# Kernel optimization log

Measured on AMD Instinct MI355X. Metric: run time of the kernel, lower is better.

Reference implementation:

```python
import jax, jax.numpy as jnp
import numpy as np

B, N, T = 8192, 100, 64  # batch, ROI nodes, BOLD timepoints/features
GCN_DIMS = [(T, 32), (32, 16), (16, 8), (8, 4), (4, 2)]
EPS = 1e-5


def _kaiming(key, fout, fin):
    return jax.random.normal(key, (fout, fin), jnp.float32) * np.float32(np.sqrt(2.0 / fin))


def setup_inputs() -> dict:
    key = jax.random.key(0)
    ks = jax.random.split(key, 10)
    inp = {"BOLD_signals": jax.random.normal(ks[0], (B, N, T), jnp.float32)}
    inp["Wq"] = _kaiming(ks[1], 32, 64); inp["bq"] = jnp.zeros((32,), jnp.float32)
    inp["Wk"] = _kaiming(ks[2], 32, 64); inp["bk"] = jnp.zeros((32,), jnp.float32)
    inp["Wv"] = _kaiming(ks[3], 32, 64); inp["bv"] = jnp.zeros((32,), jnp.float32)
    for i, (fin, fout) in enumerate(GCN_DIMS):
        inp[f"W{i+1}"] = _kaiming(ks[4 + i], fout, fin)
        inp[f"b{i+1}"] = jnp.zeros((fout,), jnp.float32)
    inp["Wf"] = _kaiming(ks[9], 2, 200); inp["bf"] = jnp.zeros((2,), jnp.float32)
    return inp


def _corrcoef_batched(feat):
    # feat: [B, N, D]; rows are variables -> [B, N, N] correlation (torch.corrcoef, clipped)
    xc = feat - feat.mean(axis=-1, keepdims=True)
    cov = jnp.einsum('bnd,bmd->bnm', xc, xc)  # unnormalized; divisor cancels
    d = jnp.sqrt(jnp.einsum('bnn->bn', cov))
    corr = cov / (d[:, :, None] * d[:, None, :])
    return jnp.clip(corr, -1.0, 1.0)


def _batchnorm_nodes(h):
    # BatchNorm1d(100) on [B, 100, C]: normalize per node over (batch, feature) dims;
    # gamma=1, beta=0 per the module's constant init; training-mode batch stats.
    mean = h.mean(axis=(0, 2), keepdims=True)
    var = ((h - mean) ** 2).mean(axis=(0, 2), keepdims=True)
    return (h - mean) * jax.lax.rsqrt(var + EPS)


def _gcn(corr, h, W, b):
    z = jnp.einsum('bnm,bmf->bnf', corr, h) @ W.T + b
    return jnp.tanh(_batchnorm_nodes(z))


def reference(BOLD_signals, Wq, bq, Wk, bk, Wv, bv,
              W1, b1, W2, b2, W3, b3, W4, b4, W5, b5, Wf, bf):
    x = BOLD_signals
    Q = x @ Wq.T + bq
    K = x @ Wk.T + bk
    V = x @ Wv.T + bv
    A = jax.nn.softmax(jnp.einsum('bnd,bmd->bnm', Q, K) / 32.0, axis=2)
    feat = jnp.einsum('bnm,bmd->bnd', A, V)  # [B, N, 32]
    corr = _corrcoef_batched(feat)           # [B, N, N]
    h = x
    for (W, b) in [(W1, b1), (W2, b2), (W3, b3), (W4, b4), (W5, b5)]:
        h = _gcn(corr, h, W, b)
    out = h.reshape(h.shape[0], -1) @ Wf.T + bf  # [B, 2]
    return out
```

## Files before the change

kernel.cpp:

```cpp
#include <hip/hip_runtime.h>
#include <hip/hip_bf16.h>


typedef unsigned int u32;
typedef unsigned short u16;
typedef float f32x4 __attribute__((ext_vector_type(4)));
typedef short s16x8 __attribute__((ext_vector_type(8)));

__device__ __forceinline__ f32x4 mfma16(s16x8 a, s16x8 b, f32x4 c) {
  return __builtin_amdgcn_mfma_f32_16x16x32_bf16(a, b, c, 0, 0, 0);
}
__device__ __forceinline__ u16 f2b(float f) {
  __hip_bfloat16 h = __float2bfloat16(f);
  u16 u; __builtin_memcpy(&u, &h, 2); return u;
}
__device__ __forceinline__ float b2f(u16 u) { return __uint_as_float((u32)u << 16); }
__device__ __forceinline__ float blo(u32 u) { return __uint_as_float(u << 16); }
__device__ __forceinline__ float bhi(u32 u) { return __uint_as_float(u & 0xffff0000u); }
__device__ __forceinline__ u32 pack_hi2(float a, float b) { return (u32)f2b(a) | ((u32)f2b(b) << 16); }
__device__ __forceinline__ u32 pack_lo2(float a, float b) {
  return (u32)f2b(a - b2f(f2b(a))) | ((u32)f2b(b - b2f(f2b(b))) << 16);
}
__device__ __forceinline__ float fast_tanh(float x) {
  float e = __expf(2.0f * x);
  return 1.0f - 2.0f * __builtin_amdgcn_rcpf(e + 1.0f);
}

#define KA_XHI_B   0
#define KA_XLO_B   16128
#define KA_A_B     0
#define KA_QS_B    32256
#define KA_KS_B    40320
#define KA_CHH_B   32256
#define KA_CHL_B   40320
#define KA_VT_B    48384
#define KA_CRH_B   0
#define KA_CRL_B   30464
#define KA_T0H_B   60928
#define KA_T0L_B   69632
#define KA_SMEM_B  78336

__global__ __launch_bounds__(512, 4) void ka_kernel(
    const float* __restrict__ x,
    const float* __restrict__ Wq, const float* __restrict__ bq,
    const float* __restrict__ Wk, const float* __restrict__ bk,
    const float* __restrict__ Wv, const float* __restrict__ bv,
    const float* __restrict__ W1, const float* __restrict__ b1,
    __hip_bfloat16* __restrict__ corr_g,
    float* __restrict__ z1g,
    float* __restrict__ stats1)
{
  __shared__ __align__(16) char smem[KA_SMEM_B];
  u16* xh  = (u16*)(smem + KA_XHI_B);
  u16* xl  = (u16*)(smem + KA_XLO_B);
  u16* A16 = (u16*)(smem + KA_A_B);
  u16* Qs  = (u16*)(smem + KA_QS_B);
  u16* Ks  = (u16*)(smem + KA_KS_B);
  u16* chh = (u16*)(smem + KA_CHH_B);
  u16* chl = (u16*)(smem + KA_CHL_B);
  u16* Vt  = (u16*)(smem + KA_VT_B);
  u16* crh = (u16*)(smem + KA_CRH_B);
  u16* crl = (u16*)(smem + KA_CRL_B);
  u16* t0h = (u16*)(smem + KA_T0H_B);
  u16* t0l = (u16*)(smem + KA_T0L_B);

  const int b = blockIdx.x, tid = threadIdx.x;
  const int w = tid >> 6, l15 = tid & 15, g = (tid & 63) >> 4;
  const f32x4 zero4 = {0.f, 0.f, 0.f, 0.f};

  float t0r[28];
  float cr[7][4];

  {
    const float2* xg2 = (const float2*)(x + (size_t)b * 6400);
    for (int i = tid; i < 112 * 32; i += 512) {
      int r = i >> 5, c2 = i & 31;
      float vx = 0.f, vy = 0.f;
      if (r < 100) { float2 v = xg2[r * 32 + c2]; vx = v.x; vy = v.y; }
      ((u32*)xh)[r * 36 + c2] = pack_hi2(vx, vy);
      ((u32*)xl)[r * 36 + c2] = pack_lo2(vx, vy);
    }
    if (tid < 256) {
      int j = tid >> 3, ii = tid & 7;
      ((u32*)Vt)[j * 68 + 56 + ii] = 0;
    }
  }
  __syncthreads();

  {
    const int mi = w >> 1, half = w & 1;
    const int j = 16 * half + l15;
    const float* Wp = (mi == 0) ? Wq : (mi == 1) ? Wk : (mi == 2) ? Wv : W1;
    float bias = (mi == 0) ? bq[j] : (mi == 1) ? bk[j] : (mi == 2) ? bv[j] : 0.f;
    s16x8 bhf[2], blf[2];
#pragma unroll
    for (int kt = 0; kt < 2; ++kt) {
      const float* wr = Wp + j * 64 + kt * 32 + g * 8;
#pragma unroll
      for (int e = 0; e < 8; ++e) {
        float wv = wr[e];
        u16 hh = f2b(wv);
        bhf[kt][e] = (short)hh;
        blf[kt][e] = (short)f2b(wv - b2f(hh));
      }
    }
#pragma unroll
    for (int tm = 0; tm < 7; ++tm) {
      f32x4 acc = zero4;
#pragma unroll
      for (int kt = 0; kt < 2; ++kt) {
        s16x8 ah = *(const s16x8*)&xh[(16 * tm + l15) * 72 + kt * 32 + g * 8];
        s16x8 al = *(const s16x8*)&xl[(16 * tm + l15) * 72 + kt * 32 + g * 8];
        acc = mfma16(al, bhf[kt], acc);
        acc = mfma16(ah, blf[kt], acc);
        acc = mfma16(ah, bhf[kt], acc);
      }
      const int row0 = 16 * tm + 4 * g;
#pragma unroll
      for (int r = 0; r < 4; ++r) {
        int row = row0 + r;
        float v = acc[r] + bias;
        if (mi == 0)      Qs[row * 36 + j] = f2b(v);
        else if (mi == 1) Ks[row * 36 + j] = f2b(v);
        else if (mi == 2) Vt[j * 136 + row] = f2b(v);
        else              t0r[tm * 4 + r] = v;
      }
    }
  }
  __syncthreads();

  if (w < 7) {
    const int tm = w;
    s16x8 aq = *(const s16x8*)&Qs[(16 * tm + l15) * 36 + g * 8];
    f32x4 sc[7];
#pragma unroll
    for (int tn = 0; tn < 7; ++tn) {
      s16x8 bb = *(const s16x8*)&Ks[(16 * tn + l15) * 36 + g * 8];
      sc[tn] = mfma16(aq, bb, zero4);
    }
    const int row0 = 16 * tm + 4 * g;
#pragma unroll
    for (int r = 0; r < 4; ++r) {
      const int row = row0 + r;
      float v[7];
#pragma unroll
      for (int tn = 0; tn < 7; ++tn) v[tn] = sc[tn][r];
      if (l15 >= 4) v[6] = -3.0e38f;
      float m = v[0];
#pragma unroll
      for (int tn = 1; tn < 7; ++tn) m = fmaxf(m, v[tn]);
#pragma unroll
      for (int off = 1; off < 16; off <<= 1) m = fmaxf(m, __shfl_xor(m, off, 16));
      float e[7], s = 0.f;
#pragma unroll
      for (int tn = 0; tn < 7; ++tn) { e[tn] = __expf((v[tn] - m) * 0.03125f); s += e[tn]; }
#pragma unroll
      for (int off = 1; off < 16; off <<= 1) s += __shfl_xor(s, off, 16);
      float rr = __builtin_amdgcn_rcpf(s);
      bool ok = row < 100;
#pragma unroll
      for (int tn = 0; tn < 7; ++tn) {
        float a = ok ? e[tn] * rr : 0.f;
        A16[row * 136 + 16 * tn + l15] = f2b(a);
      }
      if (l15 < 8) ((u32*)A16)[row * 68 + 56 + l15] = 0;
    }
  }
  __syncthreads();

  if (w < 7) {
    const int tm = w;
    f32x4 f0 = zero4, f1 = zero4;
#pragma unroll
    for (int kt = 0; kt < 4; ++kt) {
      s16x8 a   = *(const s16x8*)&A16[(16 * tm + l15) * 136 + kt * 32 + g * 8];
      s16x8 b0  = *(const s16x8*)&Vt[l15 * 136 + kt * 32 + g * 8];
      s16x8 b1v = *(const s16x8*)&Vt[(16 + l15) * 136 + kt * 32 + g * 8];
      f0 = mfma16(a, b0, f0);
      f1 = mfma16(a, b1v, f1);
    }
    const int row0 = 16 * tm + 4 * g;
#pragma unroll
    for (int r = 0; r < 4; ++r) {
      float v0 = f0[r], v1 = f1[r];
      float s = v0 + v1;
#pragma unroll
      for (int off = 1; off < 16; off <<= 1) s += __shfl_xor(s, off, 16);
      float mean = s * 0.03125f;
      float xc0 = v0 - mean, xc1 = v1 - mean;
      float q = xc0 * xc0 + xc1 * xc1;
#pragma unroll
      for (int off = 1; off < 16; off <<= 1) q += __shfl_xor(q, off, 16);
      float inv = rsqrtf(q + 1e-30f);
      const int row = row0 + r;
      float c0 = xc0 * inv, c1 = xc1 * inv;
      u16 h0 = f2b(c0), h1 = f2b(c1);
      chh[row * 36 + l15]      = h0;
      chh[row * 36 + 16 + l15] = h1;
      chl[row * 36 + l15]      = f2b(c0 - b2f(h0));
      chl[row * 36 + 16 + l15] = f2b(c1 - b2f(h1));
    }
  }
  __syncthreads();

  if (w < 7) {
    u16* cgu = (u16*)(corr_g + (size_t)b * 10000);
    const int tm = w;
    s16x8 ah = *(const s16x8*)&chh[(16 * tm + l15) * 36 + g * 8];
    s16x8 al = *(const s16x8*)&chl[(16 * tm + l15) * 36 + g * 8];
    const int row0 = 16 * tm + 4 * g;
#pragma unroll
    for (int tn = 0; tn < 7; ++tn) {
      s16x8 bh = *(const s16x8*)&chh[(16 * tn + l15) * 36 + g * 8];
      s16x8 bl = *(const s16x8*)&chl[(16 * tn + l15) * 36 + g * 8];
      f32x4 c = mfma16(al, bh, zero4);
      c = mfma16(ah, bl, c);
      c = mfma16(ah, bh, c);
      const int col = 16 * tn + l15;
#pragma unroll
      for (int r = 0; r < 4; ++r) {
        float d = fminf(1.f, fmaxf(-1.f, c[r]));
        cr[tn][r] = d;
        const int row = row0 + r;
        if (row < 100 && col < 100) cgu[row * 100 + col] = f2b(d);
      }
    }
  }
  __syncthreads();

  {
    if (w < 7) {
      const int tm = w;
      const int row0 = 16 * tm + 4 * g;
#pragma unroll
      for (int r = 0; r < 4; ++r) {
        const int row = row0 + r;
#pragma unroll
        for (int tn = 0; tn < 7; ++tn) {
          const int col = 16 * tn + l15;
          float d = cr[tn][r];
          u16 hh = f2b(d);
          crh[row * 136 + col] = hh;
          crl[row * 136 + col] = f2b(d - b2f(hh));
        }
        if (l15 < 8) {
          ((u32*)crh)[row * 68 + 56 + l15] = 0;
          ((u32*)crl)[row * 68 + 56 + l15] = 0;
        }
      }
    }
    if (w >= 6) {
      const int j = 16 * (w & 1) + l15;
#pragma unroll
      for (int tm = 0; tm < 7; ++tm) {
#pragma unroll
        for (int r = 0; r < 4; ++r) {
          int m = 16 * tm + 4 * g + r;
          float v = t0r[tm * 4 + r];
          u16 hh = f2b(v);
          t0h[j * 136 + m] = hh;
          t0l[j * 136 + m] = f2b(v - b2f(hh));
        }
      }
      if (g == 0) {
#pragma unroll
        for (int ii = 0; ii < 8; ++ii) ((u32*)t0h)[j * 68 + 56 + ii] = 0;
      } else if (g == 1) {
#pragma unroll
        for (int ii = 0; ii < 8; ++ii) ((u32*)t0l)[j * 68 + 56 + ii] = 0;
      }
    }
  }
  __syncthreads();

  if (w < 7) {
    const int tm = w;
    float bj0 = b1[l15], bj1 = b1[16 + l15];
    float* zo = z1g + (size_t)b * 3200;
    f32x4 z0 = zero4, z1v = zero4;
#pragma unroll
    for (int kt = 0; kt < 4; ++kt) {
      s16x8 a_h = *(const s16x8*)&crh[(16 * tm + l15) * 136 + kt * 32 + g * 8];
      s16x8 a_l = *(const s16x8*)&crl[(16 * tm + l15) * 136 + kt * 32 + g * 8];
      s16x8 b0h = *(const s16x8*)&t0h[l15 * 136 + kt * 32 + g * 8];
      s16x8 b0l = *(const s16x8*)&t0l[l15 * 136 + kt * 32 + g * 8];
      s16x8 b1h = *(const s16x8*)&t0h[(16 + l15) * 136 + kt * 32 + g * 8];
      s16x8 b1l = *(const s16x8*)&t0l[(16 + l15) * 136 + kt * 32 + g * 8];
      z0 = mfma16(a_l, b0h, z0);  z0 = mfma16(a_h, b0l, z0);  z0 = mfma16(a_h, b0h, z0);
      z1v = mfma16(a_l, b1h, z1v); z1v = mfma16(a_h, b1l, z1v); z1v = mfma16(a_h, b1h, z1v);
    }
    const int row0 = 16 * tm + 4 * g;
#pragma unroll
    for (int r = 0; r < 4; ++r) {
      const int row = row0 + r;
      float v0 = z0[r] + bj0, v1 = z1v[r] + bj1;
      if (row < 100) { zo[row * 32 + l15] = v0; zo[row * 32 + 16 + l15] = v1; }
      float s = v0 + v1, ss = v0 * v0 + v1 * v1;
#pragma unroll
      for (int off = 1; off < 16; off <<= 1) {
        s += __shfl_xor(s, off, 16); ss += __shfl_xor(ss, off, 16);
      }
      if (row < 100 && l15 == 0) { atomicAdd(&stats1[row], s); atomicAdd(&stats1[100 + row], ss); }
    }
  }
}

template<int FIN, int FOUT>
__global__ __launch_bounds__(256, 3) void kb_kernel(
    const float* __restrict__ zin,
    const __hip_bfloat16* __restrict__ corr_g,
    const float* __restrict__ W, const float* __restrict__ bias,
    const float* __restrict__ stats_in, float* __restrict__ stats_out,
    float* __restrict__ zout)
{
  constexpr int LOGF  = (FOUT == 16) ? 4 : (FOUT == 8) ? 3 : (FOUT == 4) ? 2 : 1;
  constexpr int LOGFI = (FIN == 32) ? 5 : (FIN == 16) ? 4 : (FIN == 8) ? 3 : 2;
  constexpr int RP = 256 / FOUT;
  constexpr int NR = (100 + RP - 1) / RP;

  __shared__ u32 clLu[100 * 52];
  __shared__ float mS[100], vS[100];
  __shared__ float hL[100 * 33];
  __shared__ float tL[100 * (FOUT + 1)];

  const int b = blockIdx.x, tid = threadIdx.x;

  {
    const u32* cgu = (const u32*)(corr_g + (size_t)b * 10000);
    for (int i = tid; i < 5000; i += 256) {
      int n = (i * 5243) >> 18;
      int mm = i - n * 50;
      clLu[n * 52 + mm] = cgu[i];
    }
  }
  if (tid < 100) {
    float cnt  = 8192.0f * (float)FIN;
    float mean = stats_in[tid] / cnt;
    float var  = stats_in[100 + tid] / cnt - mean * mean;
    mS[tid] = mean;
    vS[tid] = rsqrtf(var + 1e-5f);
  }
  __syncthreads();

  {
    const float4* zb4 = (const float4*)(zin + (size_t)b * 100 * FIN);
    for (int i4 = tid; i4 < 25 * FIN; i4 += 256) {
      int n = i4 >> (LOGFI - 2);
      int c = (i4 << 2) & (FIN - 1);
      float4 z = zb4[i4];
      float mn = mS[n], iv = vS[n];
      hL[n * 33 + c + 0] = fast_tanh((z.x - mn) * iv);
      hL[n * 33 + c + 1] = fast_tanh((z.y - mn) * iv);
      hL[n * 33 + c + 2] = fast_tanh((z.z - mn) * iv);
      hL[n * 33 + c + 3] = fast_tanh((z.w - mn) * iv);
    }
  }
  __syncthreads();

  const int j  = tid & (FOUT - 1);
  const int nb = tid >> LOGF;

  {
    float wreg[FIN];
#pragma unroll
    for (int c = 0; c < FIN; ++c) wreg[c] = W[j * FIN + c];
#pragma unroll
    for (int k = 0; k < NR; ++k) {
      int n = nb + k * RP;
      if (n < 100) {
        float a = 0.f;
#pragma unroll
        for (int c = 0; c < FIN; ++c) a = fmaf(hL[n * 33 + c], wreg[c], a);
        tL[n * (FOUT + 1) + j] = a;
      }
    }
  }
  __syncthreads();

  {
    float acc[NR];
    float bj = bias[j];
#pragma unroll
    for (int k = 0; k < NR; ++k) acc[k] = bj;
    int nrow[NR];
#pragma unroll
    for (int k = 0; k < NR; ++k) nrow[k] = min(nb + k * RP, 99);
#pragma unroll 5
    for (int m4 = 0; m4 < 25; ++m4) {
      float ta = tL[(m4 * 4 + 0) * (FOUT + 1) + j];
      float tb = tL[(m4 * 4 + 1) * (FOUT + 1) + j];
      float tc = tL[(m4 * 4 + 2) * (FOUT + 1) + j];
      float td = tL[(m4 * 4 + 3) * (FOUT + 1) + j];
#pragma unroll
      for (int k = 0; k < NR; ++k) {
        u32 p0 = clLu[nrow[k] * 52 + 2 * m4];
        u32 p1 = clLu[nrow[k] * 52 + 2 * m4 + 1];
        acc[k] = fmaf(blo(p0), ta, fmaf(bhi(p0), tb,
                 fmaf(blo(p1), tc, fmaf(bhi(p1), td, acc[k]))));
      }
    }
    float* zo = zout + (size_t)b * 100 * FOUT;
#pragma unroll
    for (int k = 0; k < NR; ++k) {
      int n = nb + k * RP;
      if (n < 100) {
        float v = acc[k];
        zo[n * FOUT + j] = v;
        float s = v, ss = v * v;
#pragma unroll
        for (int off = FOUT >> 1; off; off >>= 1) {
          s  += __shfl_xor(s, off, FOUT);
          ss += __shfl_xor(ss, off, FOUT);
        }
        if (j == 0) {
          atomicAdd(&stats_out[n], s);
          atomicAdd(&stats_out[100 + n], ss);
        }
      }
    }
  }
}

__global__ __launch_bounds__(256) void kf_kernel(
    const float* __restrict__ z5, const float* __restrict__ stats5,
    const float* __restrict__ Wf, const float* __restrict__ bfv,
    float* __restrict__ out)
{
  __shared__ float mS[100], vS[100];
  const int tid = threadIdx.x;
  if (tid < 100) {
    float cnt  = 8192.0f * 2.0f;
    float mean = stats5[tid] / cnt;
    float var  = stats5[100 + tid] / cnt - mean * mean;
    mS[tid] = mean;
    vS[tid] = rsqrtf(var + 1e-5f);
  }
  __syncthreads();
  const int wvid = tid >> 6, lane = tid & 63;
  const int b = blockIdx.x * 4 + wvid;
  const float* zb = z5 + (size_t)b * 200;
  float a0 = 0.f, a1 = 0.f;
#pragma unroll
  for (int p = 0; p < 4; ++p) {
    int jj = lane + p * 64;
    if (jj < 200) {
      int n = jj >> 1;
      float hv = fast_tanh((zb[jj] - mS[n]) * vS[n]);
      a0 = fmaf(hv, Wf[jj], a0);
      a1 = fmaf(hv, Wf[200 + jj], a1);
    }
  }
#pragma unroll
  for (int off = 32; off; off >>= 1) {
    a0 += __shfl_xor(a0, off, 64);
    a1 += __shfl_xor(a1, off, 64);
  }
  if (lane == 0) {
    out[b * 2 + 0] = a0 + bfv[0];
    out[b * 2 + 1] = a1 + bfv[1];
  }
}

extern "C" void kernel_launch(void* const* d_in, const int* in_sizes, int n_in,
                              void* d_out, int out_size, void* d_ws, size_t ws_size,
                              hipStream_t stream)
{
  const float* x  = (const float*)d_in[0];
  const float* Wq = (const float*)d_in[1];
  const float* bq = (const float*)d_in[2];
  const float* Wk = (const float*)d_in[3];
  const float* bk = (const float*)d_in[4];
  const float* Wv = (const float*)d_in[5];
  const float* bv = (const float*)d_in[6];
  const float* W1 = (const float*)d_in[7];
  const float* b1 = (const float*)d_in[8];
  const float* W2 = (const float*)d_in[9];
  const float* b2 = (const float*)d_in[10];
  const float* W3 = (const float*)d_in[11];
  const float* b3 = (const float*)d_in[12];
  const float* W4 = (const float*)d_in[13];
  const float* b4 = (const float*)d_in[14];
  const float* W5 = (const float*)d_in[15];
  const float* b5 = (const float*)d_in[16];
  const float* Wf = (const float*)d_in[17];
  const float* bf = (const float*)d_in[18];
  float* out = (float*)d_out;

  char* ws = (char*)d_ws;
  const size_t NEED = 321130400ull;
  if (ws_size < NEED) return;

  __hip_bfloat16* corr_g = (__hip_bfloat16*)ws;
  float* zA    = (float*)(ws + 163840000ull);
  float* zB    = (float*)(ws + 268697600ull);
  float* stats = (float*)(ws + 321126400ull);

  (void)hipMemsetAsync(stats, 0, 5 * 200 * sizeof(float), stream);

  ka_kernel<<<8192, 512, 0, stream>>>(x, Wq, bq, Wk, bk, Wv, bv, W1, b1,
                                      corr_g, zA, stats);
  kb_kernel<32, 16><<<8192, 256, 0, stream>>>(zA, corr_g, W2, b2, stats,       stats + 200, zB);
  kb_kernel<16,  8><<<8192, 256, 0, stream>>>(zB, corr_g, W3, b3, stats + 200, stats + 400, zA);
  kb_kernel< 8,  4><<<8192, 256, 0, stream>>>(zA, corr_g, W4, b4, stats + 400, stats + 600, zB);
  kb_kernel< 4,  2><<<8192, 256, 0, stream>>>(zB, corr_g, W5, b5, stats + 600, stats + 800, zA);
  kf_kernel<<<2048, 256, 0, stream>>>(zA, stats + 800, Wf, bf, out);
}
```

Before: 3.858 ms.

## Split first GCN layer out of attention kernel to shrink LDS and raise occupancy

The first GCN layer (x@W1 then corr@t) moves out of the attention/correlation kernel into a new kb0 kernel that uses fp32 FMA with a bf16 correlation matrix, like the later layers. The attention kernel no longer stages x in LDS; it converts x to hi/lo bf16 straight from global memory, and its LDS footprint and row padding shrink so more blocks can be resident. Padding of the corr LDS rows in kb kernels goes from 52 to 50 and launch bounds rise. The trade is an extra kernel launch, an extra read of corr and x, lower precision for layer 1 (bf16 corr instead of the hi/lo split), and possible LDS bank conflicts from the tighter strides.

```diff
diff --git a/kernel.cpp b/kernel.cpp
--- a/kernel.cpp
+++ b/kernel.cpp
@@ -17,100 +17,73 @@
 __device__ __forceinline__ float b2f(u16 u) { return __uint_as_float((u32)u << 16); }
 __device__ __forceinline__ float blo(u32 u) { return __uint_as_float(u << 16); }
 __device__ __forceinline__ float bhi(u32 u) { return __uint_as_float(u & 0xffff0000u); }
-__device__ __forceinline__ u32 pack_hi2(float a, float b) { return (u32)f2b(a) | ((u32)f2b(b) << 16); }
-__device__ __forceinline__ u32 pack_lo2(float a, float b) {
-  return (u32)f2b(a - b2f(f2b(a))) | ((u32)f2b(b - b2f(f2b(b))) << 16);
-}
 __device__ __forceinline__ float fast_tanh(float x) {
   float e = __expf(2.0f * x);
   return 1.0f - 2.0f * __builtin_amdgcn_rcpf(e + 1.0f);
 }
-
-#define KA_XHI_B   0
-#define KA_XLO_B   16128
-#define KA_A_B     0
-#define KA_QS_B    32256
-#define KA_KS_B    40320
-#define KA_CHH_B   32256
-#define KA_CHL_B   40320
-#define KA_VT_B    48384
-#define KA_CRH_B   0
-#define KA_CRL_B   30464
-#define KA_T0H_B   60928
-#define KA_T0L_B   69632
-#define KA_SMEM_B  78336
-
-__global__ __launch_bounds__(512, 4) void ka_kernel(
+__device__ __forceinline__ void hilo8(const float* p, bool ok, s16x8& hi, s16x8& lo) {
+  const float4* p4 = (const float4*)p;
+  float4 a = {0.f,0.f,0.f,0.f}, b = {0.f,0.f,0.f,0.f};
+  if (ok) { a = p4[0]; b = p4[1]; }
+  float v[8] = {a.x,a.y,a.z,a.w,b.x,b.y,b.z,b.w};
+#pragma unroll
+  for (int e = 0; e < 8; ++e) {
+    u16 hh = f2b(v[e]);
+    hi[e] = (short)hh;
+    lo[e] = (short)f2b(v[e] - b2f(hh));
+  }
+}
+
+#define KA_QS_B   0
+#define KA_KS_B   8064
+#define KA_CHH_B  0
+#define KA_CHL_B  8064
+#define KA_A_B    16128
+#define KA_VT_B   45696
+#define KA_SMEM_B 54144
+
+__global__ __launch_bounds__(512, 6) void ka_kernel(
     const float* __restrict__ x,
     const float* __restrict__ Wq, const float* __restrict__ bq,
     const float* __restrict__ Wk, const float* __restrict__ bk,
     const float* __restrict__ Wv, const float* __restrict__ bv,
-    const float* __restrict__ W1, const float* __restrict__ b1,
-    __hip_bfloat16* __restrict__ corr_g,
-    float* __restrict__ z1g,
-    float* __restrict__ stats1)
+    __hip_bfloat16* __restrict__ corr_g)
 {
   __shared__ __align__(16) char smem[KA_SMEM_B];
-  u16* xh  = (u16*)(smem + KA_XHI_B);
-  u16* xl  = (u16*)(smem + KA_XLO_B);
-  u16* A16 = (u16*)(smem + KA_A_B);
   u16* Qs  = (u16*)(smem + KA_QS_B);
   u16* Ks  = (u16*)(smem + KA_KS_B);
   u16* chh = (u16*)(smem + KA_CHH_B);
   u16* chl = (u16*)(smem + KA_CHL_B);
+  u16* A16 = (u16*)(smem + KA_A_B);
   u16* Vt  = (u16*)(smem + KA_VT_B);
-  u16* crh = (u16*)(smem + KA_CRH_B);
-  u16* crl = (u16*)(smem + KA_CRL_B);
-  u16* t0h = (u16*)(smem + KA_T0H_B);
-  u16* t0l = (u16*)(smem + KA_T0L_B);
 
   const int b = blockIdx.x, tid = threadIdx.x;
   const int w = tid >> 6, l15 = tid & 15, g = (tid & 63) >> 4;
   const f32x4 zero4 = {0.f, 0.f, 0.f, 0.f};
 
-  float t0r[28];
-  float cr[7][4];
-
-  {
-    const float2* xg2 = (const float2*)(x + (size_t)b * 6400);
-    for (int i = tid; i < 112 * 32; i += 512) {
-      int r = i >> 5, c2 = i & 31;
-      float vx = 0.f, vy = 0.f;
-      if (r < 100) { float2 v = xg2[r * 32 + c2]; vx = v.x; vy = v.y; }
-      ((u32*)xh)[r * 36 + c2] = pack_hi2(vx, vy);
-      ((u32*)xl)[r * 36 + c2] = pack_lo2(vx, vy);
-    }
-    if (tid < 256) {
-      int j = tid >> 3, ii = tid & 7;
-      ((u32*)Vt)[j * 68 + 56 + ii] = 0;
-    }
-  }
-  __syncthreads();
-
-  {
+  if (tid < 256) {
+    int j = tid >> 3, ii = tid & 7;
+    ((u32*)Vt)[j * 66 + 56 + ii] = 0;
+  }
+
+  if (w < 6) {
     const int mi = w >> 1, half = w & 1;
     const int j = 16 * half + l15;
-    const float* Wp = (mi == 0) ? Wq : (mi == 1) ? Wk : (mi == 2) ? Wv : W1;
-    float bias = (mi == 0) ? bq[j] : (mi == 1) ? bk[j] : (mi == 2) ? bv[j] : 0.f;
+    const float* Wp = (mi == 0) ? Wq : (mi == 1) ? Wk : Wv;
+    float bias = (mi == 0) ? bq[j] : (mi == 1) ? bk[j] : bv[j];
     s16x8 bhf[2], blf[2];
 #pragma unroll
-    for (int kt = 0; kt < 2; ++kt) {
-      const float* wr = Wp + j * 64 + kt * 32 + g * 8;
-#pragma unroll
-      for (int e = 0; e < 8; ++e) {
-        float wv = wr[e];
-        u16 hh = f2b(wv);
-        bhf[kt][e] = (short)hh;
-        blf[kt][e] = (short)f2b(wv - b2f(hh));
-      }
-    }
+    for (int kt = 0; kt < 2; ++kt)
+      hilo8(Wp + j * 64 + kt * 32 + g * 8, true, bhf[kt], blf[kt]);
+    const float* xb = x + (size_t)b * 6400;
 #pragma unroll
     for (int tm = 0; tm < 7; ++tm) {
+      const int arow = 16 * tm + l15;
       f32x4 acc = zero4;
 #pragma unroll
       for (int kt = 0; kt < 2; ++kt) {
-        s16x8 ah = *(const s16x8*)&xh[(16 * tm + l15) * 72 + kt * 32 + g * 8];
-        s16x8 al = *(const s16x8*)&xl[(16 * tm + l15) * 72 + kt * 32 + g * 8];
+        s16x8 ah, al;
+        hilo8(xb + arow * 64 + kt * 32 + g * 8, arow < 100, ah, al);
         acc = mfma16(al, bhf[kt], acc);
         acc = mfma16(ah, blf[kt], acc);
         acc = mfma16(ah, bhf[kt], acc);
@@ -122,8 +95,7 @@
         float v = acc[r] + bias;
         if (mi == 0)      Qs[row * 36 + j] = f2b(v);
         else if (mi == 1) Ks[row * 36 + j] = f2b(v);
-        else if (mi == 2) Vt[j * 136 + row] = f2b(v);
-        else              t0r[tm * 4 + r] = v;
+        else              Vt[j * 132 + row] = f2b(v);
       }
     }
   }
@@ -161,9 +133,9 @@
 #pragma unroll
       for (int tn = 0; tn < 7; ++tn) {
         float a = ok ? e[tn] * rr : 0.f;
-        A16[row * 136 + 16 * tn + l15] = f2b(a);
-      }
-      if (l15 < 8) ((u32*)A16)[row * 68 + 56 + l15] = 0;
+        A16[row * 132 + 16 * tn + l15] = f2b(a);
+      }
+      if (l15 < 8) ((u32*)A16)[row * 66 + 56 + l15] = 0;
     }
   }
   __syncthreads();
@@ -173,9 +145,9 @@
     f32x4 f0 = zero4, f1 = zero4;
 #pragma unroll
     for (int kt = 0; kt < 4; ++kt) {
-      s16x8 a   = *(const s16x8*)&A16[(16 * tm + l15) * 136 + kt * 32 + g * 8];
-      s16x8 b0  = *(const s16x8*)&Vt[l15 * 136 + kt * 32 + g * 8];
-      s16x8 b1v = *(const s16x8*)&Vt[(16 + l15) * 136 + kt * 32 + g * 8];
+      s16x8 a   = *(const s16x8*)&A16[(16 * tm + l15) * 132 + kt * 32 + g * 8];
+      s16x8 b0  = *(const s16x8*)&Vt[l15 * 132 + kt * 32 + g * 8];
+      s16x8 b1v = *(const s16x8*)&Vt[(16 + l15) * 132 + kt * 32 + g * 8];
       f0 = mfma16(a, b0, f0);
       f1 = mfma16(a, b1v, f1);
     }
@@ -217,96 +189,113 @@
       c = mfma16(ah, bl, c);
       c = mfma16(ah, bh, c);
       const int col = 16 * tn + l15;
-#pragma unroll
-      for (int r = 0; r < 4; ++r) {
-        float d = fminf(1.f, fmaxf(-1.f, c[r]));
-        cr[tn][r] = d;
-        const int row = row0 + r;
-        if (row < 100 && col < 100) cgu[row * 100 + col] = f2b(d);
-      }
-    }
-  }
-  __syncthreads();
-
-  {
-    if (w < 7) {
-      const int tm = w;
-      const int row0 = 16 * tm + 4 * g;
-#pragma unroll
-      for (int r = 0; r < 4; ++r) {
-        const int row = row0 + r;
-#pragma unroll
-        for (int tn = 0; tn < 7; ++tn) {
-          const int col = 16 * tn + l15;
-          float d = cr[tn][r];
-          u16 hh = f2b(d);
-          crh[row * 136 + col] = hh;
-          crl[row * 136 + col] = f2b(d - b2f(hh));
-        }
-        if (l15 < 8) {
-          ((u32*)crh)[row * 68 + 56 + l15] = 0;
-          ((u32*)crl)[row * 68 + 56 + l15] = 0;
-        }
-      }
-    }
-    if (w >= 6) {
-      const int j = 16 * (w & 1) + l15;
-#pragma unroll
-      for (int tm = 0; tm < 7; ++tm) {
+      if (col < 100) {
 #pragma unroll
         for (int r = 0; r < 4; ++r) {
-          int m = 16 * tm + 4 * g + r;
-          float v = t0r[tm * 4 + r];
-          u16 hh = f2b(v);
-          t0h[j * 136 + m] = hh;
-          t0l[j * 136 + m] = f2b(v - b2f(hh));
-        }
-      }
-      if (g == 0) {
-#pragma unroll
-        for (int ii = 0; ii < 8; ++ii) ((u32*)t0h)[j * 68 + 56 + ii] = 0;
-      } else if (g == 1) {
-#pragma unroll
-        for (int ii = 0; ii < 8; ++ii) ((u32*)t0l)[j * 68 + 56 + ii] = 0;
-      }
-    }
-  }
-  __syncthreads();
-
-  if (w < 7) {
-    const int tm = w;
-    float bj0 = b1[l15], bj1 = b1[16 + l15];
-    float* zo = z1g + (size_t)b * 3200;
-    f32x4 z0 = zero4, z1v = zero4;
-#pragma unroll
-    for (int kt = 0; kt < 4; ++kt) {
-      s16x8 a_h = *(const s16x8*)&crh[(16 * tm + l15) * 136 + kt * 32 + g * 8];
-      s16x8 a_l = *(const s16x8*)&crl[(16 * tm + l15) * 136 + kt * 32 + g * 8];
-      s16x8 b0h = *(const s16x8*)&t0h[l15 * 136 + kt * 32 + g * 8];
-      s16x8 b0l = *(const s16x8*)&t0l[l15 * 136 + kt * 32 + g * 8];
-      s16x8 b1h = *(const s16x8*)&t0h[(16 + l15) * 136 + kt * 32 + g * 8];
-      s16x8 b1l = *(const s16x8*)&t0l[(16 + l15) * 136 + kt * 32 + g * 8];
-      z0 = mfma16(a_l, b0h, z0);  z0 = mfma16(a_h, b0l, z0);  z0 = mfma16(a_h, b0h, z0);
-      z1v = mfma16(a_l, b1h, z1v); z1v = mfma16(a_h, b1l, z1v); z1v = mfma16(a_h, b1h, z1v);
-    }
-    const int row0 = 16 * tm + 4 * g;
-#pragma unroll
-    for (int r = 0; r < 4; ++r) {
-      const int row = row0 + r;
-      float v0 = z0[r] + bj0, v1 = z1v[r] + bj1;
-      if (row < 100) { zo[row * 32 + l15] = v0; zo[row * 32 + 16 + l15] = v1; }
-      float s = v0 + v1, ss = v0 * v0 + v1 * v1;
-#pragma unroll
-      for (int off = 1; off < 16; off <<= 1) {
-        s += __shfl_xor(s, off, 16); ss += __shfl_xor(ss, off, 16);
-      }
-      if (row < 100 && l15 == 0) { atomicAdd(&stats1[row], s); atomicAdd(&stats1[100 + row], ss); }
+          const int row = row0 + r;
+          if (row < 100)
+            cgu[row * 100 + col] = f2b(fminf(1.f, fmaxf(-1.f, c[r])));
+        }
+      }
+    }
+  }
+}
+
+__global__ __launch_bounds__(256, 4) void kb0_kernel(
+    const float* __restrict__ x,
+    const __hip_bfloat16* __restrict__ corr_g,
+    const float* __restrict__ W1, const float* __restrict__ b1,
+    float* __restrict__ stats_out,
+    float* __restrict__ zout)
+{
+  __shared__ u32 clLu[100 * 50];
+  __shared__ float tL[100 * 33];
+
+  const int b = blockIdx.x, tid = threadIdx.x;
+
+  {
+    const u32* cgu = (const u32*)(corr_g + (size_t)b * 10000);
+    for (int i = tid; i < 5000; i += 256) {
+      int n = (i * 5243) >> 18;
+      int mm = i - n * 50;
+      clLu[n * 50 + mm] = cgu[i];
+    }
+  }
+
+  const int j  = tid & 31;
+  const int nb = tid >> 5;
+
+  {
+    float wreg[64];
+#pragma unroll
+    for (int c = 0; c < 64; ++c) wreg[c] = W1[j * 64 + c];
+    const float* xb = x + (size_t)b * 6400;
+#pragma unroll
+    for (int k = 0; k < 13; ++k) {
+      int n = nb + k * 8;
+      if (n < 100) {
+        const float4* xr = (const float4*)(xb + n * 64);
+        float a = 0.f;
+#pragma unroll
+        for (int c4 = 0; c4 < 16; ++c4) {
+          float4 xv = xr[c4];
+          a = fmaf(xv.x, wreg[c4 * 4 + 0], a);
+          a = fmaf(xv.y, wreg[c4 * 4 + 1], a);
+          a = fmaf(xv.z, wreg[c4 * 4 + 2], a);
+          a = fmaf(xv.w, wreg[c4 * 4 + 3], a);
+        }
+        tL[n * 33 + j] = a;
+      }
+    }
+  }
+  __syncthreads();
+
+  {
+    float acc[13];
+    float bj = b1[j];
+#pragma unroll
+    for (int k = 0; k < 13; ++k) acc[k] = bj;
+    int nrow[13];
+#pragma unroll
+    for (int k = 0; k < 13; ++k) nrow[k] = min(nb + k * 8, 99);
+#pragma unroll 5
+    for (int m4 = 0; m4 < 25; ++m4) {
+      float ta = tL[(m4 * 4 + 0) * 33 + j];
+      float tb = tL[(m4 * 4 + 1) * 33 + j];
+      float tc = tL[(m4 * 4 + 2) * 33 + j];
+      float td = tL[(m4 * 4 + 3) * 33 + j];
+#pragma unroll
+      for (int k = 0; k < 13; ++k) {
+        u32 p0 = clLu[nrow[k] * 50 + 2 * m4];
+        u32 p1 = clLu[nrow[k] * 50 + 2 * m4 + 1];
+        acc[k] = fmaf(blo(p0), ta, fmaf(bhi(p0), tb,
+                 fmaf(blo(p1), tc, fmaf(bhi(p1), td, acc[k]))));
+      }
+    }
+    float* zo = zout + (size_t)b * 3200;
+#pragma unroll
+    for (int k = 0; k < 13; ++k) {
+      int n = nb + k * 8;
+      if (n < 100) {
+        float v = acc[k];
+        zo[n * 32 + j] = v;
+        float s = v, ss = v * v;
+#pragma unroll
+        for (int off = 16; off; off >>= 1) {
+          s  += __shfl_xor(s, off, 32);
+          ss += __shfl_xor(ss, off, 32);
+        }
+        if (j == 0) {
+          atomicAdd(&stats_out[n], s);
+          atomicAdd(&stats_out[100 + n], ss);
+        }
+      }
     }
   }
 }
 
 template<int FIN, int FOUT>
-__global__ __launch_bounds__(256, 3) void kb_kernel(
+__global__ __launch_bounds__(256, 4) void kb_kernel(
     const float* __restrict__ zin,
     const __hip_bfloat16* __restrict__ corr_g,
     const float* __restrict__ W, const float* __restrict__ bias,
@@ -318,7 +307,7 @@
   constexpr int RP = 256 / FOUT;
   constexpr int NR = (100 + RP - 1) / RP;
 
-  __shared__ u32 clLu[100 * 52];
+  __shared__ u32 clLu[100 * 50];
   __shared__ float mS[100], vS[100];
   __shared__ float hL[100 * 33];
   __shared__ float tL[100 * (FOUT + 1)];
@@ -330,7 +319,7 @@
     for (int i = tid; i < 5000; i += 256) {
       int n = (i * 5243) >> 18;
       int mm = i - n * 50;
-      clLu[n * 52 + mm] = cgu[i];
+      clLu[n * 50 + mm] = cgu[i];
     }
   }
   if (tid < 100) {
@@ -393,8 +382,8 @@
       float td = tL[(m4 * 4 + 3) * (FOUT + 1) + j];
 #pragma unroll
       for (int k = 0; k < NR; ++k) {
-        u32 p0 = clLu[nrow[k] * 52 + 2 * m4];
-        u32 p1 = clLu[nrow[k] * 52 + 2 * m4 + 1];
+        u32 p0 = clLu[nrow[k] * 50 + 2 * m4];
+        u32 p1 = clLu[nrow[k] * 50 + 2 * m4 + 1];
         acc[k] = fmaf(blo(p0), ta, fmaf(bhi(p0), tb,
                  fmaf(blo(p1), tc, fmaf(bhi(p1), td, acc[k]))));
       }
@@ -497,8 +486,8 @@
 
   (void)hipMemsetAsync(stats, 0, 5 * 200 * sizeof(float), stream);
 
-  ka_kernel<<<8192, 512, 0, stream>>>(x, Wq, bq, Wk, bk, Wv, bv, W1, b1,
-                                      corr_g, zA, stats);
+  ka_kernel<<<8192, 512, 0, stream>>>(x, Wq, bq, Wk, bk, Wv, bv, corr_g);
+  kb0_kernel<<<8192, 256, 0, stream>>>(x, corr_g, W1, b1, stats, zA);
   kb_kernel<32, 16><<<8192, 256, 0, stream>>>(zA, corr_g, W2, b2, stats,       stats + 200, zB);
   kb_kernel<16,  8><<<8192, 256, 0, stream>>>(zB, corr_g, W3, b3, stats + 200, stats + 400, zA);
   kb_kernel< 8,  4><<<8192, 256, 0, stream>>>(zA, corr_g, W4, b4, stats + 400, stats + 600, zB);
```

New measurement: 4.313 ms. +11.8%, slower.
